# Optimization experiments

Hardware: AMD Instinct MI355X
Metric: run time of the kernel (lower is better)

Reference implementation:

```python
import jax, jax.numpy as jnp
import numpy as np

D_MODEL = 1024

def setup_inputs() -> dict:
    key = jax.random.key(0)
    k1, k2 = jax.random.split(key, 2)
    x = jax.random.normal(k1, (4, 2048, D_MODEL), dtype=jnp.float32)
    W_attn = jax.random.normal(k2, (3 * D_MODEL, D_MODEL), dtype=jnp.float32) * (1.0 / np.sqrt(D_MODEL))
    b_attn = jnp.zeros((3 * D_MODEL,), dtype=jnp.float32)
    return {"x": x, "W_attn": W_attn, "b_attn": b_attn}

def reference(x, W_attn, b_attn):
    B, T, C = x.shape
    # fused QKV projection; torch split order is (k, q, v)
    kqv = x @ W_attn.T + b_attn            # [B, T, 3C]
    k, q, v = jnp.split(kqv, 3, axis=-1)   # each [B, T, C]
    # NOTE: original computes k @ q^T (quirk), scaled by sqrt(d_model)
    scores = jnp.einsum('btc,bsc->bts', k, q) / jnp.sqrt(jnp.asarray(C, x.dtype))
    causal = jnp.tril(jnp.ones((T, T), dtype=bool))
    scores = jnp.where(causal[None, :, :], scores, -jnp.inf)
    attn = jax.nn.softmax(scores, axis=-1)
    return jnp.einsum('bts,bsc->btc', attn, v)
```

## Files before the change

### kernel.cpp

```cpp
#include <hip/hip_runtime.h>

typedef __bf16 bf16x8 __attribute__((ext_vector_type(8)));
typedef float f32x4 __attribute__((ext_vector_type(4)));
typedef float fl4 __attribute__((ext_vector_type(4)));
typedef unsigned short us4 __attribute__((ext_vector_type(4)));
typedef unsigned short us8 __attribute__((ext_vector_type(8)));

__device__ __forceinline__ unsigned short f2bf(float f) {
  unsigned u = __builtin_bit_cast(unsigned, f);
  u += 0x7fffu + ((u >> 16) & 1u);
  return (unsigned short)(u >> 16);
}
__device__ __forceinline__ float bf2f(unsigned short h) {
  unsigned u = ((unsigned)h) << 16;
  return __builtin_bit_cast(float, u);
}

__device__ __forceinline__ void async16(const void* g, void* l) {
  __builtin_amdgcn_global_load_lds(
      (const __attribute__((address_space(1))) unsigned int*)g,
      (__attribute__((address_space(3))) unsigned int*)l, 16, 0, 0);
}

#define BARM() asm volatile("s_barrier" ::: "memory")
#define VMCNT3() asm volatile("s_waitcnt vmcnt(3)" ::: "memory")
#define VMCNT4() asm volatile("s_waitcnt vmcnt(4)" ::: "memory")
#define VMCNT8() asm volatile("s_waitcnt vmcnt(8)" ::: "memory")
#define LGKM0() asm volatile("s_waitcnt lgkmcnt(0)" ::: "memory")
#define LGKM8() asm volatile("s_waitcnt lgkmcnt(8)" ::: "memory")
#define SCHEDB() __builtin_amdgcn_sched_barrier(0)

__global__ __launch_bounds__(256) void cvt_bf16_2(const float* __restrict__ sA,
                                                  unsigned short* __restrict__ dA, int nA,
                                                  const float* __restrict__ sB,
                                                  unsigned short* __restrict__ dB, int nB) {
  int i = blockIdx.x * 256 + threadIdx.x;
  const float* s;
  unsigned short* d;
  if (i < nA) {
    s = sA; d = dA;
  } else {
    i -= nA;
    if (i >= nB) return;
    s = sB; d = dB;
  }
  fl4 f = ((const fl4*)s)[i];
  us4 o;
  o[0] = f2bf(f[0]); o[1] = f2bf(f[1]); o[2] = f2bf(f[2]); o[3] = f2bf(f[3]);
  ((us4*)d)[i] = o;
}

__global__ __launch_bounds__(256) void transpose_v(const unsigned short* __restrict__ kqv,
                                                   unsigned short* __restrict__ vT) {
  int b = blockIdx.z;
  int t0 = blockIdx.x * 64;
  int c0 = blockIdx.y * 64;
  __shared__ unsigned short tile[64][68];
  int tid = threadIdx.x;
#pragma unroll
  for (int i = 0; i < 4; ++i) {
    int idx = i * 256 + tid;
    int r = idx >> 4;
    int c4 = (idx & 15) * 4;
    const unsigned short* src = kqv + ((size_t)(b * 2048 + t0 + r)) * 3072 + 2048 + c0 + c4;
    us4 v = *(const us4*)src;
    *(us4*)&tile[r][c4] = v;
  }
  __syncthreads();
#pragma unroll
  for (int i = 0; i < 4; ++i) {
    int idx = i * 256 + tid;
    int rc = idx >> 4;
    int t4 = (idx & 15) * 4;
    us4 v;
    v[0] = tile[t4 + 0][rc]; v[1] = tile[t4 + 1][rc];
    v[2] = tile[t4 + 2][rc]; v[3] = tile[t4 + 3][rc];
    unsigned short* dst = vT + ((size_t)(b * 1024 + c0 + rc)) * 2048 + t0 + t4;
    *(us4*)dst = v;
  }
}

__global__ __launch_bounds__(512, 2) void gemm_g0(
    const unsigned short* __restrict__ A, const unsigned short* __restrict__ B,
    unsigned short* __restrict__ C, const float* __restrict__ bias) {
  const int flat = blockIdx.x;
  const int swz = (flat & 7) * 32 + (flat >> 3);
  const int bx = swz >> 5;
  const int by = swz & 31;
  const int rowBase = by * 256, colBase = bx * 384;
  const int lda = 1024, ldc = 3072, nk = 32;

  __shared__ __align__(16) unsigned char lds[81920];
  const int tid = threadIdx.x;
  const int lane = tid & 63, wid = tid >> 6;
  const int wr = wid >> 2, wc = wid & 3;
  const int l15 = lane & 15, l4 = lane >> 4;

  f32x4 acc[8][6] = {};
  bf16x8 af0[4], af1[4], bf[6];

  const unsigned short* Ab = A + (size_t)rowBase * lda;
  const unsigned short* Bb = B + (size_t)colBase * lda;
  unsigned aoff[2], boff[3], aldso[2], bldso[3];
#pragma unroll
  for (int i = 0; i < 3; ++i) {
    int off = i * 8192 + tid * 16;
    int r = off >> 6;
    int sb = ((off >> 4) & 3) ^ ((r >> 1) & 3);
    if (i < 2) { aoff[i] = (unsigned)(r * lda + sb * 8); aldso[i] = (unsigned)off; }
    boff[i] = (unsigned)(r * lda + sb * 8);
    bldso[i] = (unsigned)off;
  }

  auto STA = [&](int buf, int op, int koff) {
    async16(Ab + (size_t)(aoff[op] + (unsigned)koff), lds + buf * 40960 + aldso[op]);
  };
  auto STB = [&](int buf, int op, int koff) {
    async16(Bb + (size_t)(boff[op] + (unsigned)koff),
            lds + buf * 40960 + 16384 + bldso[op]);
  };
  auto RA = [&](int buf, int m) -> bf16x8 {
    int row = wr * 128 + m * 16 + l15;
    return *(const bf16x8*)(lds + buf * 40960 + row * 64 +
                            (((l4 ^ (row >> 1)) & 3) * 16));
  };
  auto RB = [&](int buf, int n) -> bf16x8 {
    int row = wc * 96 + n * 16 + l15;
    return *(const bf16x8*)(lds + buf * 40960 + 16384 + row * 64 +
                            (((l4 ^ (row >> 1)) & 3) * 16));
  };

#define RD_A03(BUF) _Pragma("unroll") for (int mi = 0; mi < 4; ++mi) af0[mi] = RA((BUF), mi)
#define RD_A47(BUF) _Pragma("unroll") for (int mi = 0; mi < 4; ++mi) af1[mi] = RA((BUF), 4 + mi)
#define RD_B02(BUF) _Pragma("unroll") for (int nj = 0; nj < 3; ++nj) bf[nj] = RB((BUF), nj)
#define RD_B35(BUF) _Pragma("unroll") for (int nj = 0; nj < 3; ++nj) bf[3 + nj] = RB((BUF), 3 + nj)

#define MQ(MB, NB, AF)                                                         \
  _Pragma("unroll") for (int mi = 0; mi < 4; ++mi)                             \
  _Pragma("unroll") for (int nj = 0; nj < 3; ++nj)                             \
      acc[(MB) + mi][(NB) + nj] = __builtin_amdgcn_mfma_f32_16x16x32_bf16(     \
          AF[mi], bf[(NB) + nj], acc[(MB) + mi][(NB) + nj], 0, 0, 0)

#define PHASE(RDS, STG, GATE, MB, NB, AF)                                      \
  do {                                                                         \
    RDS;                                                                       \
    STG;                                                                       \
    BARM();                                                                    \
    LGKM0();                                                                   \
    SCHEDB();                                                                  \
    __builtin_amdgcn_s_setprio(1);                                             \
    MQ(MB, NB, AF);                                                            \
    __builtin_amdgcn_s_setprio(0);                                             \
    GATE;                                                                      \
    BARM();                                                                    \
  } while (0)

  STA(0, 0, 0); STA(0, 1, 0);
#pragma unroll
  for (int i = 0; i < 3; ++i) STB(0, i, 0);
#pragma unroll
  for (int i = 0; i < 3; ++i) STB(1, i, 32);
  VMCNT3();
  BARM();

  for (int it = 0; it < 16; ++it) {
    int t = it * 2;
    int kA1 = (t + 1) * 32;
    int k2 = (t + 2 < nk - 1 ? t + 2 : nk - 1) * 32;
    int k3 = (t + 3 < nk - 1 ? t + 3 : nk - 1) * 32;
    PHASE({ RD_A03(0); RD_B02(0); }, { STA(1, 0, kA1); STA(1, 1, kA1); },
          (void)0, 0, 0, af0);
    PHASE({ RD_B35(0); }, (void)0, (void)0, 0, 3, af0);
    PHASE({ RD_A47(0); }, { STB(0, 0, k2); STB(0, 1, k2); STB(0, 2, k2); },
          (void)0, 4, 3, af1);
    PHASE({}, (void)0, VMCNT3(), 4, 0, af1);
    PHASE({ RD_A03(1); RD_B02(1); }, { STA(0, 0, k2); STA(0, 1, k2); },
          (void)0, 0, 0, af0);
    PHASE({ RD_B35(1); }, (void)0, (void)0, 0, 3, af0);
    PHASE({ RD_A47(1); }, { STB(1, 0, k3); STB(1, 1, k3); STB(1, 2, k3); },
          (void)0, 4, 3, af1);
    PHASE({}, (void)0, VMCNT3(), 4, 0, af1);
  }
#undef PHASE
#undef MQ
#undef RD_A03
#undef RD_A47
#undef RD_B02
#undef RD_B35

  const int cr = l4 * 4;
#pragma unroll
  for (int n = 0; n < 6; ++n) {
    int col = colBase + wc * 96 + n * 16 + l15;
    float bv = bias[col];
#pragma unroll
    for (int m = 0; m < 8; ++m) {
      int row = rowBase + wr * 128 + m * 16 + cr;
#pragma unroll
      for (int i = 0; i < 4; ++i)
        C[(size_t)(row + i) * ldc + col] = f2bf(acc[m][n][i] + bv);
    }
  }
}

__global__ __launch_bounds__(512, 2) void gemm_s(
    const unsigned short* __restrict__ A, int lda, long long sA,
    const unsigned short* __restrict__ B, int ldb, long long sB,
    unsigned short* __restrict__ C, int ldc, long long sC,
    float scale, int K) {
  int bx = blockIdx.x, by = blockIdx.y;
  const int bz = blockIdx.z;
  if (bx > by) return;
  A += (size_t)bz * sA;
  B += (size_t)bz * sB;
  const int rowBase = by * 256;
  const int colBase = bx * 256;
  const int nk = K / 64;

  __shared__ __align__(16) unsigned char lds[131072];
  const int tid = threadIdx.x;
  const int lane = tid & 63;
  const int wid = tid >> 6;
  const int wr = wid >> 2;
  const int wc = wid & 3;
  const int l15 = lane & 15, l4 = lane >> 4, l7 = lane & 7;

  f32x4 acc[8][4] = {};
  bf16x8 af0[4][2], af1[4][2], bf0[2][2], bf1[2][2];

  const unsigned short* Ab = A + (size_t)rowBase * lda;
  const unsigned short* Bb = B + (size_t)colBase * ldb;
  unsigned loff[2][2];
  unsigned lldso[2];
#pragma unroll
  for (int i = 0; i < 2; ++i) {
    int off = (i * 512 + tid) * 16;
    int r = off >> 7;
    int sb = ((off >> 4) & 7) ^ (r & 7);
    lldso[i] = (unsigned)off;
#pragma unroll
    for (int hh = 0; hh < 2; ++hh)
      loff[hh][i] = (unsigned)((hh * 128 + r) * lda + sb * 8);
  }

  auto STAGE = [&](int bufc, int isB, int half, const unsigned short* Gb, int koff) {
#pragma unroll
    for (int i = 0; i < 2; ++i)
      async16(Gb + (size_t)(loff[half][i] + (unsigned)koff),
              lds + bufc * 65536 + isB * 32768 + half * 16384 + lldso[i]);
  };
  auto RDA = [&](int bufc, int m, int kk) -> bf16x8 {
    int row = m * 16 + l15;
    int blk = (kk * 4 + l4) ^ l7;
    return *(const bf16x8*)(lds + bufc * 65536 + wr * 16384 + row * 128 + blk * 16);
  };
  auto RDB = [&](int bufc, int n, int kk) -> bf16x8 {
    int row = (wc & 1) * 64 + n * 16 + l15;
    int blk = (kk * 4 + l4) ^ l7;
    return *(const bf16x8*)(lds + bufc * 65536 + 32768 + (wc >> 1) * 16384 +
                            row * 128 + blk * 16);
  };

#define RDA8(dst, BUF, Q)                                                      \
  _Pragma("unroll") for (int mi = 0; mi < 4; ++mi)                             \
  _Pragma("unroll") for (int kk = 0; kk < 2; ++kk)                             \
      dst[mi][kk] = RDA((BUF), (Q) * 4 + mi, kk)
#define RDB4(dst, BUF, NB)                                                     \
  _Pragma("unroll") for (int nj = 0; nj < 2; ++nj)                             \
  _Pragma("unroll") for (int kk = 0; kk < 2; ++kk)                             \
      dst[nj][kk] = RDB((BUF), (NB) + nj, kk)

#define MFMAQ(MB, NB, AF, BF)                                                  \
  _Pragma("unroll") for (int kk = 0; kk < 2; ++kk)                             \
  _Pragma("unroll") for (int mi = 0; mi < 4; ++mi)                             \
  _Pragma("unroll") for (int nj = 0; nj < 2; ++nj)                             \
      acc[(MB) + mi][(NB) + nj] = __builtin_amdgcn_mfma_f32_16x16x32_bf16(     \
          AF[mi][kk], BF[nj][kk], acc[(MB) + mi][(NB) + nj], 0, 0, 0)

#define PH(RDS, STG, HINT, GATE, MB, NB, AF, BF)                               \
  do {                                                                         \
    RDS;                                                                       \
    STG;                                                                       \
    HINT;                                                                      \
    BARM();                                                                    \
    LGKM0();                                                                   \
    SCHEDB();                                                                  \
    __builtin_amdgcn_s_setprio(1);                                             \
    MFMAQ(MB, NB, AF, BF);                                                     \
    __builtin_amdgcn_s_setprio(0);                                             \
    GATE;                                                                      \
    BARM();                                                                    \
  } while (0)

  STAGE(0, 0, 0, Ab, 0);
  STAGE(0, 0, 1, Ab, 0);
  STAGE(0, 1, 0, Bb, 0);
  STAGE(0, 1, 1, Bb, 0);
  STAGE(1, 1, 0, Bb, 64);
  STAGE(1, 1, 1, Bb, 64);
  VMCNT4();
  BARM();

  const int nt2 = nk >> 1;
  for (int it = 0; it < nt2; ++it) {
    int t = it * 2;
    int kA1 = (t + 1) * 64;
    int k2 = (t + 2 < nk - 1 ? t + 2 : nk - 1) * 64;
    int k3 = (t + 3 < nk - 1 ? t + 3 : nk - 1) * 64;
    PH({ RDA8(af0, 0, 0); RDB4(bf0, 0, 0); }, STAGE(1, 0, 0, Ab, kA1), LGKM8(),
       (void)0, 0, 0, af0, bf0);
    PH({ RDB4(bf1, 0, 2); }, STAGE(1, 0, 1, Ab, kA1), (void)0,
       (void)0, 0, 2, af0, bf1);
    PH({ RDA8(af1, 0, 1); }, STAGE(0, 1, 0, Bb, k2), (void)0,
       (void)0, 4, 2, af1, bf1);
    PH({}, STAGE(0, 1, 1, Bb, k2), (void)0,
       VMCNT4(), 4, 0, af1, bf0);
    PH({ RDA8(af0, 1, 0); RDB4(bf0, 1, 0); }, STAGE(0, 0, 0, Ab, k2), LGKM8(),
       (void)0, 0, 0, af0, bf0);
    PH({ RDB4(bf1, 1, 2); }, STAGE(0, 0, 1, Ab, k2), (void)0,
       (void)0, 0, 2, af0, bf1);
    PH({ RDA8(af1, 1, 1); }, STAGE(1, 1, 0, Bb, k3), (void)0,
       (void)0, 4, 2, af1, bf1);
    PH({}, STAGE(1, 1, 1, Bb, k3), (void)0,
       VMCNT4(), 4, 0, af1, bf0);
  }
#undef PH
#undef MFMAQ
#undef RDA8
#undef RDB4

  const int cr = l4 * 4;
  unsigned short* Cb = C + (size_t)bz * sC;
#pragma unroll
  for (int n = 0; n < 4; ++n) {
    int col = colBase + wc * 64 + n * 16 + l15;
#pragma unroll
    for (int m = 0; m < 8; ++m) {
      int row = rowBase + wr * 128 + m * 16 + cr;
#pragma unroll
      for (int i = 0; i < 4; ++i)
        Cb[(size_t)(row + i) * ldc + col] = f2bf(acc[m][n][i] * scale);
    }
  }
}

__global__ __launch_bounds__(256, 2) void gemm_pv2(
    const unsigned short* __restrict__ S, const unsigned short* __restrict__ V,
    float* __restrict__ O) {
  const int f = blockIdx.x;
  const int bx = f & 7;
  const int p = (f >> 3) & 7;
  const int bz = f >> 6;
  const int byH = 15 - p;
  const int nkL = 2 * (p + 1);
  const int nkH = 32 - 2 * p;
  const unsigned short* base = S + (size_t)bz * 2048 * 2048;
  const unsigned short* AH = base + (size_t)(byH * 128) * 2048;
  const unsigned short* AL = base + (size_t)(p * 128) * 2048;
  const unsigned short* Bb = V + (size_t)bz * 1024 * 2048 + (size_t)(bx * 128) * 2048;
  float* Ob = O + (size_t)bz * 2048 * 1024;

  __shared__ __align__(16) unsigned char lds[65536];
  const int tid = threadIdx.x;
  const int lane = tid & 63, wid = tid >> 6;
  const int wr = (wid >> 1) * 64, wc = (wid & 1) * 64;
  const int l15 = lane & 15, l4 = lane >> 4, l7 = lane & 7;

  f32x4 accH[4][4] = {}, accL[4][4] = {};

  unsigned goff[4], ldso[4];
#pragma unroll
  for (int ii = 0; ii < 4; ++ii) {
    int off = (ii * 256 + tid) * 16;
    int rr = off >> 7;
    int sb = ((off >> 4) & 7) ^ (rr & 7);
    goff[ii] = (unsigned)(rr * 2048 + sb * 8);
    ldso[ii] = (unsigned)off;
  }

  auto ST = [&](int buf, const unsigned short* Ap, unsigned kof) {
#pragma unroll
    for (int ii = 0; ii < 4; ++ii) {
      async16(Ap + (size_t)(goff[ii] + kof), lds + buf * 32768 + ldso[ii]);
      async16(Bb + (size_t)(goff[ii] + kof), lds + buf * 32768 + 16384 + ldso[ii]);
    }
  };
  auto ITEM = [&](int i, const unsigned short*& P, unsigned& kf) {
    if (i < 2 * nkL) {
      P = (i & 1) ? AL : AH;
      kf = (unsigned)((i >> 1) * 64);
    } else {
      P = AH;
      kf = (unsigned)((i - nkL) * 64);
    }
  };

#define PVSTEP(BUF, ACC, NITEM)                                                \
  do {                                                                         \
    const unsigned short* nP;                                                  \
    unsigned nK;                                                               \
    ITEM((NITEM) < 33 ? (NITEM) : 33, nP, nK);                                 \
    VMCNT8();                                                                  \
    BARM();                                                                    \
    bf16x8 af[4][2], bfr[4][2];                                                \
    _Pragma("unroll") for (int m = 0; m < 4; ++m) {                            \
      int row = wr + m * 16 + l15;                                             \
      _Pragma("unroll") for (int kk = 0; kk < 2; ++kk)                         \
        af[m][kk] = *(const bf16x8*)(lds + (BUF) * 32768 + row * 128 +         \
                                     (((kk * 4 + l4) ^ l7) * 16));             \
    }                                                                          \
    _Pragma("unroll") for (int n = 0; n < 4; ++n) {                            \
      int row = wc + n * 16 + l15;                                             \
      _Pragma("unroll") for (int kk = 0; kk < 2; ++kk)                         \
        bfr[n][kk] = *(const bf16x8*)(lds + (BUF) * 32768 + 16384 + row * 128 +\
                                      (((kk * 4 + l4) ^ l7) * 16));            \
    }                                                                          \
    LGKM0();                                                                   \
    BARM();                                                                    \
    ST((BUF), nP, nK);                                                         \
    SCHEDB();                                                                  \
    __builtin_amdgcn_s_setprio(1);                                             \
    _Pragma("unroll") for (int kk = 0; kk < 2; ++kk)                           \
    _Pragma("unroll") for (int m = 0; m < 4; ++m)                              \
    _Pragma("unroll") for (int n = 0; n < 4; ++n)                              \
      ACC[m][n] = __builtin_amdgcn_mfma_f32_16x16x32_bf16(af[m][kk], bfr[n][kk],\
                                                          ACC[m][n], 0, 0, 0); \
    __builtin_amdgcn_s_setprio(0);                                             \
  } while (0)

  ST(0, AH, 0);
  {
    const unsigned short* P; unsigned kf;
    ITEM(1, P, kf);
    ST(1, P, kf);
  }

  for (int t = 0; t < nkL; ++t) {
    PVSTEP(0, accH, 2 * t + 2);
    PVSTEP(1, accL, 2 * t + 3);
  }
  for (int u = nkL; u < nkH; u += 2) {
    PVSTEP(0, accH, u + nkL + 2);
    PVSTEP(1, accH, u + nkL + 3);
  }
#undef PVSTEP

  const int cr = l4 * 4;
#pragma unroll
  for (int n = 0; n < 4; ++n) {
    int col = bx * 128 + wc + n * 16 + l15;
#pragma unroll
    for (int m = 0; m < 4; ++m) {
      int rH = byH * 128 + wr + m * 16 + cr;
      int rL = p * 128 + wr + m * 16 + cr;
#pragma unroll
      for (int i = 0; i < 4; ++i) {
        Ob[(size_t)(rH + i) * 1024 + col] = accH[m][n][i];
        Ob[(size_t)(rL + i) * 1024 + col] = accL[m][n][i];
      }
    }
  }
}

__global__ __launch_bounds__(256) void softmax_causal(unsigned short* __restrict__ S) {
  const int T = 2048;
  int t = blockIdx.x, b = blockIdx.y;
  unsigned short* row = S + ((size_t)b * T + t) * T;
  const int nv = t + 1;
  const int bound = ((t >> 7) + 1) << 7;
  int tid = threadIdx.x;
  int lane = tid & 63, wid = tid >> 6;
  int s0 = tid * 8;
  us8 raw = {};
  if (s0 < nv) raw = *(const us8*)(row + s0);
  float v[8];
  float m = -3.0e38f;
#pragma unroll
  for (int j = 0; j < 8; ++j) {
    v[j] = bf2f(raw[j]);
    if (s0 + j < nv) m = fmaxf(m, v[j]);
  }
#pragma unroll
  for (int o = 32; o > 0; o >>= 1) m = fmaxf(m, __shfl_xor(m, o, 64));
  __shared__ float red[4];
  if (lane == 0) red[wid] = m;
  __syncthreads();
  m = fmaxf(fmaxf(red[0], red[1]), fmaxf(red[2], red[3]));
  __syncthreads();
  float sum = 0.f;
#pragma unroll
  for (int j = 0; j < 8; ++j) {
    float e = (s0 + j < nv) ? exp2f(v[j] - m) : 0.f;
    v[j] = e;
    sum += e;
  }
#pragma unroll
  for (int o = 32; o > 0; o >>= 1) sum += __shfl_xor(sum, o, 64);
  if (lane == 0) red[wid] = sum;
  __syncthreads();
  sum = red[0] + red[1] + red[2] + red[3];
  float inv = 1.0f / sum;
  if (s0 < bound) {
    us8 outv;
#pragma unroll
    for (int j = 0; j < 8; ++j) outv[j] = f2bf(v[j] * inv);
    *(us8*)(row + s0) = outv;
  }
}

extern "C" void kernel_launch(void* const* d_in, const int* in_sizes, int n_in,
                              void* d_out, int out_size, void* d_ws, size_t ws_size,
                              hipStream_t stream) {
  const float* x = (const float*)d_in[0];
  const float* W = (const float*)d_in[1];
  const float* bias = (const float*)d_in[2];
  float* out = (float*)d_out;

  char* ws = (char*)d_ws;
  if (ws_size < 106954752u) return;
  unsigned short* xbf = (unsigned short*)(ws);
  unsigned short* vT = xbf;
  unsigned short* wbf = (unsigned short*)(ws + 16777216);
  unsigned short* kqv = (unsigned short*)(ws + 23068672);
  unsigned short* S = (unsigned short*)(ws + 73400320);

  const float kSoftmaxScale = 1.4426950408889634f / 32.0f;

  cvt_bf16_2<<<11264, 256, 0, stream>>>(x, xbf, 2097152, W, wbf, 786432);

  gemm_g0<<<dim3(256, 1, 1), 512, 0, stream>>>(xbf, wbf, kqv, bias);

  transpose_v<<<dim3(32, 16, 4), 256, 0, stream>>>(kqv, vT);

  gemm_s<<<dim3(8, 8, 4), 512, 0, stream>>>(
      kqv, 3072, 2048LL * 3072, kqv + 1024, 3072, 2048LL * 3072,
      S, 2048, 2048LL * 2048, kSoftmaxScale, 1024);

  softmax_causal<<<dim3(2048, 4), 256, 0, stream>>>(S);

  gemm_pv2<<<dim3(256, 1, 1), 256, 0, stream>>>(S, vT, out);
}
```

Measured before the change: 177.6 us.

## Retile QKV GEMM to 256x192 tiles with K=64 stages and 512 blocks

The QKV projection GEMM now uses 256x192 output tiles instead of 256x384, with K staged 64 wide and half as many iterations. The grid doubles to 512 blocks to fill more compute units, and the LDS swizzle changes to an 8-way XOR over 128-byte rows. Each wave's accumulators fall from 48 to 24 fragments, which relieves register pressure. The cost is a larger LDS footprint (112KB), which likely limits occupancy to one block per CU, and lower arithmetic intensity per tile.

```diff
diff --git a/kernel.cpp b/kernel.cpp
--- a/kernel.cpp
+++ b/kernel.cpp
@@ -84,64 +84,64 @@
     const unsigned short* __restrict__ A, const unsigned short* __restrict__ B,
     unsigned short* __restrict__ C, const float* __restrict__ bias) {
   const int flat = blockIdx.x;
-  const int swz = (flat & 7) * 32 + (flat >> 3);
+  const int swz = (flat & 7) * 64 + (flat >> 3);
   const int bx = swz >> 5;
   const int by = swz & 31;
-  const int rowBase = by * 256, colBase = bx * 384;
-  const int lda = 1024, ldc = 3072, nk = 32;
-
-  __shared__ __align__(16) unsigned char lds[81920];
+  const int rowBase = by * 256, colBase = bx * 192;
+  const int lda = 1024, ldc = 3072, nk = 16;
+
+  __shared__ __align__(16) unsigned char lds[114688];
   const int tid = threadIdx.x;
   const int lane = tid & 63, wid = tid >> 6;
   const int wr = wid >> 2, wc = wid & 3;
-  const int l15 = lane & 15, l4 = lane >> 4;
-
-  f32x4 acc[8][6] = {};
-  bf16x8 af0[4], af1[4], bf[6];
+  const int l15 = lane & 15, l4 = lane >> 4, l7 = lane & 7;
+
+  f32x4 acc[8][3] = {};
+  bf16x8 a0[4], a1[4], a2[4], a3[4], bb0[3], bb1[3];
 
   const unsigned short* Ab = A + (size_t)rowBase * lda;
   const unsigned short* Bb = B + (size_t)colBase * lda;
-  unsigned aoff[2], boff[3], aldso[2], bldso[3];
-#pragma unroll
-  for (int i = 0; i < 3; ++i) {
+  unsigned aoff[4], boff[3], aldso[4], bldso[3];
+#pragma unroll
+  for (int i = 0; i < 4; ++i) {
     int off = i * 8192 + tid * 16;
-    int r = off >> 6;
-    int sb = ((off >> 4) & 3) ^ ((r >> 1) & 3);
-    if (i < 2) { aoff[i] = (unsigned)(r * lda + sb * 8); aldso[i] = (unsigned)off; }
-    boff[i] = (unsigned)(r * lda + sb * 8);
-    bldso[i] = (unsigned)off;
+    int r = off >> 7;
+    int sb = ((off >> 4) & 7) ^ (r & 7);
+    aoff[i] = (unsigned)(r * lda + sb * 8);
+    aldso[i] = (unsigned)off;
+    if (i < 3) { boff[i] = aoff[i]; bldso[i] = (unsigned)off; }
   }
 
   auto STA = [&](int buf, int op, int koff) {
-    async16(Ab + (size_t)(aoff[op] + (unsigned)koff), lds + buf * 40960 + aldso[op]);
+    async16(Ab + (size_t)(aoff[op] + (unsigned)koff), lds + buf * 57344 + aldso[op]);
   };
   auto STB = [&](int buf, int op, int koff) {
     async16(Bb + (size_t)(boff[op] + (unsigned)koff),
-            lds + buf * 40960 + 16384 + bldso[op]);
-  };
-  auto RA = [&](int buf, int m) -> bf16x8 {
+            lds + buf * 57344 + 32768 + bldso[op]);
+  };
+  auto RA = [&](int buf, int m, int kk) -> bf16x8 {
     int row = wr * 128 + m * 16 + l15;
-    return *(const bf16x8*)(lds + buf * 40960 + row * 64 +
-                            (((l4 ^ (row >> 1)) & 3) * 16));
-  };
-  auto RB = [&](int buf, int n) -> bf16x8 {
-    int row = wc * 96 + n * 16 + l15;
-    return *(const bf16x8*)(lds + buf * 40960 + 16384 + row * 64 +
-                            (((l4 ^ (row >> 1)) & 3) * 16));
-  };
-
-#define RD_A03(BUF) _Pragma("unroll") for (int mi = 0; mi < 4; ++mi) af0[mi] = RA((BUF), mi)
-#define RD_A47(BUF) _Pragma("unroll") for (int mi = 0; mi < 4; ++mi) af1[mi] = RA((BUF), 4 + mi)
-#define RD_B02(BUF) _Pragma("unroll") for (int nj = 0; nj < 3; ++nj) bf[nj] = RB((BUF), nj)
-#define RD_B35(BUF) _Pragma("unroll") for (int nj = 0; nj < 3; ++nj) bf[3 + nj] = RB((BUF), 3 + nj)
-
-#define MQ(MB, NB, AF)                                                         \
+    int blk = (kk * 4 + l4) ^ l7;
+    return *(const bf16x8*)(lds + buf * 57344 + row * 128 + blk * 16);
+  };
+  auto RB = [&](int buf, int n, int kk) -> bf16x8 {
+    int row = wc * 48 + n * 16 + l15;
+    int blk = (kk * 4 + l4) ^ l7;
+    return *(const bf16x8*)(lds + buf * 57344 + 32768 + row * 128 + blk * 16);
+  };
+
+#define RDA4(dst, BUF, MH, KK)                                                 \
+  _Pragma("unroll") for (int mi = 0; mi < 4; ++mi) dst[mi] = RA((BUF), (MH) * 4 + mi, (KK))
+#define RDB3(dst, BUF, KK)                                                     \
+  _Pragma("unroll") for (int nj = 0; nj < 3; ++nj) dst[nj] = RB((BUF), nj, (KK))
+
+#define MQ(MB, AF, BF)                                                         \
   _Pragma("unroll") for (int mi = 0; mi < 4; ++mi)                             \
   _Pragma("unroll") for (int nj = 0; nj < 3; ++nj)                             \
-      acc[(MB) + mi][(NB) + nj] = __builtin_amdgcn_mfma_f32_16x16x32_bf16(     \
-          AF[mi], bf[(NB) + nj], acc[(MB) + mi][(NB) + nj], 0, 0, 0)
-
-#define PHASE(RDS, STG, GATE, MB, NB, AF)                                      \
+      acc[(MB) + mi][nj] = __builtin_amdgcn_mfma_f32_16x16x32_bf16(            \
+          AF[mi], BF[nj], acc[(MB) + mi][nj], 0, 0, 0)
+
+#define PHASE(RDS, STG, GATE, MB, AF, BF)                                      \
   do {                                                                         \
     RDS;                                                                       \
     STG;                                                                       \
@@ -149,49 +149,50 @@
     LGKM0();                                                                   \
     SCHEDB();                                                                  \
     __builtin_amdgcn_s_setprio(1);                                             \
-    MQ(MB, NB, AF);                                                            \
+    MQ(MB, AF, BF);                                                            \
     __builtin_amdgcn_s_setprio(0);                                             \
     GATE;                                                                      \
     BARM();                                                                    \
   } while (0)
 
-  STA(0, 0, 0); STA(0, 1, 0);
+#pragma unroll
+  for (int i = 0; i < 4; ++i) STA(0, i, 0);
 #pragma unroll
   for (int i = 0; i < 3; ++i) STB(0, i, 0);
 #pragma unroll
-  for (int i = 0; i < 3; ++i) STB(1, i, 32);
+  for (int i = 0; i < 3; ++i) STB(1, i, 64);
   VMCNT3();
   BARM();
 
-  for (int it = 0; it < 16; ++it) {
+  for (int it = 0; it < 8; ++it) {
     int t = it * 2;
-    int kA1 = (t + 1) * 32;
-    int k2 = (t + 2 < nk - 1 ? t + 2 : nk - 1) * 32;
-    int k3 = (t + 3 < nk - 1 ? t + 3 : nk - 1) * 32;
-    PHASE({ RD_A03(0); RD_B02(0); }, { STA(1, 0, kA1); STA(1, 1, kA1); },
-          (void)0, 0, 0, af0);
-    PHASE({ RD_B35(0); }, (void)0, (void)0, 0, 3, af0);
-    PHASE({ RD_A47(0); }, { STB(0, 0, k2); STB(0, 1, k2); STB(0, 2, k2); },
-          (void)0, 4, 3, af1);
-    PHASE({}, (void)0, VMCNT3(), 4, 0, af1);
-    PHASE({ RD_A03(1); RD_B02(1); }, { STA(0, 0, k2); STA(0, 1, k2); },
-          (void)0, 0, 0, af0);
-    PHASE({ RD_B35(1); }, (void)0, (void)0, 0, 3, af0);
-    PHASE({ RD_A47(1); }, { STB(1, 0, k3); STB(1, 1, k3); STB(1, 2, k3); },
-          (void)0, 4, 3, af1);
-    PHASE({}, (void)0, VMCNT3(), 4, 0, af1);
+    int kA1 = (t + 1) * 64;
+    int k2 = (t + 2 < nk - 1 ? t + 2 : nk - 1) * 64;
+    int k3 = (t + 3 < nk - 1 ? t + 3 : nk - 1) * 64;
+    PHASE({ RDA4(a0, 0, 0, 0); RDB3(bb0, 0, 0); }, { STA(1, 0, kA1); STA(1, 1, kA1); },
+          (void)0, 0, a0, bb0);
+    PHASE({ RDA4(a1, 0, 0, 1); RDB3(bb1, 0, 1); }, { STA(1, 2, kA1); STA(1, 3, kA1); },
+          (void)0, 0, a1, bb1);
+    PHASE({ RDA4(a2, 0, 1, 0); }, { STB(0, 0, k2); STB(0, 1, k2); STB(0, 2, k2); },
+          (void)0, 4, a2, bb0);
+    PHASE({ RDA4(a3, 0, 1, 1); }, (void)0, VMCNT3(), 4, a3, bb1);
+    PHASE({ RDA4(a0, 1, 0, 0); RDB3(bb0, 1, 0); }, { STA(0, 0, k2); STA(0, 1, k2); },
+          (void)0, 0, a0, bb0);
+    PHASE({ RDA4(a1, 1, 0, 1); RDB3(bb1, 1, 1); }, { STA(0, 2, k2); STA(0, 3, k2); },
+          (void)0, 0, a1, bb1);
+    PHASE({ RDA4(a2, 1, 1, 0); }, { STB(1, 0, k3); STB(1, 1, k3); STB(1, 2, k3); },
+          (void)0, 4, a2, bb0);
+    PHASE({ RDA4(a3, 1, 1, 1); }, (void)0, VMCNT3(), 4, a3, bb1);
   }
 #undef PHASE
 #undef MQ
-#undef RD_A03
-#undef RD_A47
-#undef RD_B02
-#undef RD_B35
+#undef RDA4
+#undef RDB3
 
   const int cr = l4 * 4;
 #pragma unroll
-  for (int n = 0; n < 6; ++n) {
-    int col = colBase + wc * 96 + n * 16 + l15;
+  for (int n = 0; n < 3; ++n) {
+    int col = colBase + wc * 48 + n * 16 + l15;
     float bv = bias[col];
 #pragma unroll
     for (int m = 0; m < 8; ++m) {
@@ -528,7 +529,7 @@
 
   cvt_bf16_2<<<11264, 256, 0, stream>>>(x, xbf, 2097152, W, wbf, 786432);
 
-  gemm_g0<<<dim3(256, 1, 1), 512, 0, stream>>>(xbf, wbf, kqv, bias);
+  gemm_g0<<<dim3(512, 1, 1), 512, 0, stream>>>(xbf, wbf, kqv, bias);
 
   transpose_v<<<dim3(32, 16, 4), 256, 0, stream>>>(kqv, vT);
 
```

Measured after the change: 169.3 us. -4.7%, faster.
